# Performance work log

Hardware: AMD Instinct MI355X
Metric: run time of the kernel (lower is better)

## Reference

```python
import jax, jax.numpy as jnp
import numpy as np

STALK_DIM = 16
N_NODES = 50000
N_EDGES = 400000
HIDDEN = 64


def setup_inputs() -> dict:
    key = jax.random.key(0)
    k1, k2, k3, k4 = jax.random.split(key, 4)
    d = STALK_DIM
    x = jax.random.normal(k1, (N_NODES, d), dtype=jnp.float32)
    edge_index = jax.random.randint(k2, (2, N_EDGES), 0, N_NODES, dtype=jnp.int64)
    W1 = jax.random.normal(k3, (HIDDEN, 2 * d), dtype=jnp.float32) * (1.0 / np.sqrt(2 * d))
    b1 = jnp.zeros((HIDDEN,), dtype=jnp.float32)
    W2 = jax.random.normal(k4, (d, HIDDEN), dtype=jnp.float32) * (1.0 / np.sqrt(HIDDEN))
    b2 = jnp.zeros((d,), dtype=jnp.float32)
    return {"x": x, "edge_index": edge_index, "W1": W1, "b1": b1, "W2": W2, "b2": b2}


def reference(x, edge_index, W1, b1, W2, b2):
    d = x.shape[1]
    n = x.shape[0]
    src, dst = edge_index[0], edge_index[1]
    xs, xd = x[src], x[dst]  # [E, d]

    def reflection(a, b):
        h = jax.nn.relu(jnp.concatenate([a, b], axis=1) @ W1.T + b1)
        return h @ W2.T + b2  # [E, d]

    def householder(v):
        # F.normalize(v, dim=1): v / max(||v||, 1e-12)
        vn = v / jnp.maximum(jnp.linalg.norm(v, axis=1, keepdims=True), 1e-12)
        return jnp.eye(d, dtype=v.dtype)[None] - 2.0 * vn[:, :, None] * vn[:, None, :]

    F_s = householder(reflection(xs, xd))  # [E, d, d]
    F_d = householder(reflection(xd, xs))  # [E, d, d]
    L_sd = -jnp.einsum('eki,ekj->eij', F_s, F_d)  # -F_s^T @ F_d, [E, d, d]

    # degrees: both endpoints of every edge contribute 1
    ones_e = jnp.ones(src.shape[0], dtype=x.dtype)
    deg = jnp.zeros(n, dtype=x.dtype).at[src].add(ones_e).at[dst].add(ones_e)
    deg_inv_sqrt = 1.0 / jnp.sqrt(jnp.maximum(deg, 1e-5))
    # D_inv_sqrt is scalar*I per node, so normalization is a scalar coefficient per edge
    coef = deg_inv_sqrt[src] * deg_inv_sqrt[dst]  # [E]

    # out[s] -= D^-1/2_s L D^-1/2_d x[d] ; out[d] -= D^-1/2_d L^T D^-1/2_s x[s]
    msg_s = coef[:, None] * jnp.einsum('eij,ej->ei', L_sd, xd)  # goes to src
    msg_d = coef[:, None] * jnp.einsum('eji,ej->ei', L_sd, xs)  # goes to dst

    out = x - jnp.zeros_like(x).at[src].add(msg_s) - jnp.zeros_like(x).at[dst].add(msg_d)
    return jax.nn.relu(out)
```

## Files before the change

kernel.cpp:

```cpp
#include <hip/hip_runtime.h>
#include <hip/hip_bf16.h>

#define N_NODES 50000
#define N_EDGES 400000
#define D 16
#define HID 64

#define SCAN_B 256
#define SCAN_G ((N_NODES + SCAN_B - 1) / SCAN_B)

typedef unsigned short ushort_t;

#define CNT4_OFF  0
#define DEG_OFF   (4 * N_NODES)
#define OFF_OFF   (5 * N_NODES)
#define CUR_OFF   (6 * N_NODES + 1)
#define BS_OFF    (7 * N_NODES + 1)
#define FLAGS_I   (BS_OFF + SCAN_G)
#define MSG_OFF_I (((FLAGS_I + 2) + 3) & ~3)
#define CSR_NEEDED_BYTES ((size_t)(MSG_OFF_I + 2 * N_EDGES * D) * 4 + 64)

#define FB_NDEG   (N_NODES)
#define FB_NACC   (N_NODES * D)
#define FB_FLAGS  (FB_NDEG + FB_NACC)

__device__ __forceinline__ float bf_bits(ushort_t us) {
    return __uint_as_float(((unsigned)us) << 16);
}
__device__ __forceinline__ ushort_t f2bf(float v) {
    unsigned u = __float_as_uint(v);
    unsigned r = (u + 0x7fffu + ((u >> 16) & 1u)) >> 16;
    return (ushort_t)r;
}
__device__ __forceinline__ float ld_f(const void* p, int idx, int f32) {
    return f32 ? ((const float*)p)[idx]
               : bf_bits(((const ushort_t*)p)[idx]);
}

__device__ __forceinline__ void load16(const void* __restrict__ p, long long base,
                                       int f32, float* o) {
    if (f32) {
        const float4* q = (const float4*)((const float*)p + base);
        float4 a = q[0], b = q[1], c = q[2], d = q[3];
        o[0]=a.x; o[1]=a.y; o[2]=a.z; o[3]=a.w;
        o[4]=b.x; o[5]=b.y; o[6]=b.z; o[7]=b.w;
        o[8]=c.x; o[9]=c.y; o[10]=c.z; o[11]=c.w;
        o[12]=d.x; o[13]=d.y; o[14]=d.z; o[15]=d.w;
    } else {
        const uint4* q = (const uint4*)((const ushort_t*)p + base);
        uint4 a = q[0], b = q[1];
        unsigned u[8] = {a.x, a.y, a.z, a.w, b.x, b.y, b.z, b.w};
#pragma unroll
        for (int k = 0; k < 8; k++) {
            o[2 * k]     = __uint_as_float(u[k] << 16);
            o[2 * k + 1] = __uint_as_float(u[k] & 0xffff0000u);
        }
    }
}

__device__ __forceinline__ void load_edge(const void* __restrict__ ei, int e, int is64,
                                          int& s, int& d) {
    if (is64) {
        const long long* p = (const long long*)ei;
        s = (int)p[e];
        d = (int)p[N_EDGES + e];
    } else {
        const int* p = (const int*)ei;
        s = p[e];
        d = p[N_EDGES + e];
    }
}

__device__ __forceinline__ void detect_flags(const void* x, const void* ei, int* flags) {
    const ushort_t* h = (const ushort_t*)x;
    int f32 = 0;
    for (int k = 0; k < 256; k++) {
        float v = bf_bits(h[k]);
        if (!(v == v) || fabsf(v) > 1.0e6f) { f32 = 1; break; }
    }
    const long long* p = (const long long*)ei;
    int i64 = 1;
    for (int k = 0; k < 16; k++) {
        long long v = p[k];
        if (v < 0 || v >= N_NODES) { i64 = 0; break; }
    }
    flags[0] = f32;
    flags[1] = i64;
}

__device__ __forceinline__ void stage_weights(
    const void* W1, const void* b1, const void* W2, const void* b2, int f32,
    float* sW1, float* sW2t, float* sb1, float* sb2)
{
    int t = threadIdx.x;
    for (int idx = t; idx < HID * 2 * D; idx += blockDim.x)
        sW1[idx] = ld_f(W1, idx, f32);
    for (int idx = t; idx < HID * D; idx += blockDim.x) {
        int j = idx / D, i = idx % D;
        sW2t[idx] = ld_f(W2, i * HID + j, f32);
    }
    if (t < HID) sb1[t] = ld_f(b1, t, f32);
    if (t < D)  sb2[t] = ld_f(b2, t, f32);
}

__device__ __forceinline__ void edge_math_v4(
    const float* __restrict__ sW1, const float* __restrict__ sW2t,
    const float* __restrict__ sb1, const float* __restrict__ sb2,
    const float* xs, const float* xd, float coef,
    float* ms, float* md)
{
    float vs[D], vd[D];
#pragma unroll
    for (int i = 0; i < D; i++) { vs[i] = sb2[i]; vd[i] = sb2[i]; }

#pragma unroll 4
    for (int j = 0; j < HID; j++) {
        float hs = sb1[j], hd = sb1[j];
        const float4* w4 = (const float4*)&sW1[j * 2 * D];
#pragma unroll
        for (int t = 0; t < 4; t++) {
            float4 wv = w4[t];
            int k = 4 * t;
            hs = fmaf(wv.x, xs[k],     hs); hd = fmaf(wv.x, xd[k],     hd);
            hs = fmaf(wv.y, xs[k + 1], hs); hd = fmaf(wv.y, xd[k + 1], hd);
            hs = fmaf(wv.z, xs[k + 2], hs); hd = fmaf(wv.z, xd[k + 2], hd);
            hs = fmaf(wv.w, xs[k + 3], hs); hd = fmaf(wv.w, xd[k + 3], hd);
        }
#pragma unroll
        for (int t = 0; t < 4; t++) {
            float4 wv = w4[4 + t];
            int k = 4 * t;
            hs = fmaf(wv.x, xd[k],     hs); hd = fmaf(wv.x, xs[k],     hd);
            hs = fmaf(wv.y, xd[k + 1], hs); hd = fmaf(wv.y, xs[k + 1], hd);
            hs = fmaf(wv.z, xd[k + 2], hs); hd = fmaf(wv.z, xs[k + 2], hd);
            hs = fmaf(wv.w, xd[k + 3], hs); hd = fmaf(wv.w, xs[k + 3], hd);
        }
        hs = fmaxf(hs, 0.0f);
        hd = fmaxf(hd, 0.0f);
        const float4* w24 = (const float4*)&sW2t[j * D];
#pragma unroll
        for (int t = 0; t < 4; t++) {
            float4 u = w24[t];
            int i = 4 * t;
            vs[i]     = fmaf(u.x, hs, vs[i]);     vd[i]     = fmaf(u.x, hd, vd[i]);
            vs[i + 1] = fmaf(u.y, hs, vs[i + 1]); vd[i + 1] = fmaf(u.y, hd, vd[i + 1]);
            vs[i + 2] = fmaf(u.z, hs, vs[i + 2]); vd[i + 2] = fmaf(u.z, hd, vd[i + 2]);
            vs[i + 3] = fmaf(u.w, hs, vs[i + 3]); vd[i + 3] = fmaf(u.w, hd, vd[i + 3]);
        }
    }

    float ns = 0.0f, nd = 0.0f;
#pragma unroll
    for (int i = 0; i < D; i++) { ns = fmaf(vs[i], vs[i], ns); nd = fmaf(vd[i], vd[i], nd); }
    float is_ = 1.0f / fmaxf(sqrtf(ns), 1e-12f);
    float id_ = 1.0f / fmaxf(sqrtf(nd), 1e-12f);
#pragma unroll
    for (int i = 0; i < D; i++) { vs[i] *= is_; vd[i] *= id_; }

    float dot1 = 0.0f;
#pragma unroll
    for (int i = 0; i < D; i++) dot1 = fmaf(vd[i], xd[i], dot1);
#pragma unroll
    for (int i = 0; i < D; i++) ms[i] = fmaf(-2.0f * dot1, vd[i], xd[i]);
    float dot2 = 0.0f;
#pragma unroll
    for (int i = 0; i < D; i++) dot2 = fmaf(vs[i], ms[i], dot2);
#pragma unroll
    for (int i = 0; i < D; i++) ms[i] = coef * fmaf(-2.0f * dot2, vs[i], ms[i]);

    float dot3 = 0.0f;
#pragma unroll
    for (int i = 0; i < D; i++) dot3 = fmaf(vs[i], xs[i], dot3);
#pragma unroll
    for (int i = 0; i < D; i++) md[i] = fmaf(-2.0f * dot3, vs[i], xs[i]);
    float dot4 = 0.0f;
#pragma unroll
    for (int i = 0; i < D; i++) dot4 = fmaf(vd[i], md[i], dot4);
#pragma unroll
    for (int i = 0; i < D; i++) md[i] = coef * fmaf(-2.0f * dot4, vd[i], md[i]);
}

__global__ void csr_init_kernel(int* __restrict__ wsI,
                                const void* __restrict__ x,
                                const void* __restrict__ ei) {
    int i = blockIdx.x * blockDim.x + threadIdx.x;
    if (i < 4 * N_NODES) wsI[CNT4_OFF + i] = 0;
    if (blockIdx.x == 0 && threadIdx.x == 0)
        detect_flags(x, ei, wsI + FLAGS_I);
}

__global__ void csr_count_kernel(const void* __restrict__ ei, int* __restrict__ wsI) {
    int i64 = wsI[FLAGS_I + 1];
    int e = blockIdx.x * blockDim.x + threadIdx.x;
    if (e >= N_EDGES) return;
    int s, d;
    load_edge(ei, e, i64, s, d);
    int r = (e & 3) * N_NODES;
    atomicAdd(&wsI[CNT4_OFF + r + s], 1);
    atomicAdd(&wsI[CNT4_OFF + r + d], 1);
}

__global__ __launch_bounds__(SCAN_B) void csr_scan1_kernel(int* __restrict__ wsI) {
    __shared__ int sm[SCAN_B];
    int t = threadIdx.x;
    int g = blockIdx.x * SCAN_B + t;
    int c = 0;
    if (g < N_NODES) {
        c = wsI[CNT4_OFF + g] + wsI[CNT4_OFF + N_NODES + g]
          + wsI[CNT4_OFF + 2 * N_NODES + g] + wsI[CNT4_OFF + 3 * N_NODES + g];
        wsI[DEG_OFF + g] = c;
    }
    sm[t] = c;
    __syncthreads();
    for (int st = SCAN_B / 2; st > 0; st >>= 1) {
        if (t < st) sm[t] += sm[t + st];
        __syncthreads();
    }
    if (t == 0) wsI[BS_OFF + blockIdx.x] = sm[0];
}

__global__ __launch_bounds__(SCAN_B) void csr_scan3_kernel(int* __restrict__ wsI) {
    __shared__ int sB[SCAN_B];
    __shared__ int sm[SCAN_B];
    int t = threadIdx.x;
    int bsv = (t < SCAN_G) ? wsI[BS_OFF + t] : 0;
    sB[t] = bsv;
    __syncthreads();
    for (int st = 1; st < SCAN_B; st <<= 1) {
        int u = (t >= st) ? sB[t - st] : 0;
        __syncthreads();
        sB[t] += u;
        __syncthreads();
    }
    int blockBase = sB[blockIdx.x] - wsI[BS_OFF + blockIdx.x];

    int g = blockIdx.x * SCAN_B + t;
    int c = (g < N_NODES) ? wsI[DEG_OFF + g] : 0;
    sm[t] = c;
    __syncthreads();
    for (int st = 1; st < SCAN_B; st <<= 1) {
        int u = (t >= st) ? sm[t - st] : 0;
        __syncthreads();
        sm[t] += u;
        __syncthreads();
    }
    int excl = sm[t] - c + blockBase;
    if (g < N_NODES) {
        wsI[OFF_OFF + g] = excl;
        wsI[CUR_OFF + g] = excl;
        if (g == N_NODES - 1) wsI[OFF_OFF + N_NODES] = excl + c;
    }
}

__global__ __launch_bounds__(256) void csr_edge_kernel(
    const void* __restrict__ x,
    const void* __restrict__ ei,
    const void* __restrict__ W1,
    const void* __restrict__ b1,
    const void* __restrict__ W2,
    const void* __restrict__ b2,
    int* __restrict__ wsI)
{
    __shared__ __align__(16) float sW1[HID * 2 * D];
    __shared__ __align__(16) float sW2t[HID * D];
    __shared__ float sb1[HID];
    __shared__ float sb2[D];

    int f32 = wsI[FLAGS_I];
    int i64 = wsI[FLAGS_I + 1];
    stage_weights(W1, b1, W2, b2, f32, sW1, sW2t, sb1, sb2);
    __syncthreads();

    int e = blockIdx.x * blockDim.x + threadIdx.x;
    if (e >= N_EDGES) return;

    int s, d;
    load_edge(ei, e, i64, s, d);

    float xs[D], xd[D];
    load16(x, (long long)s * D, f32, xs);
    load16(x, (long long)d * D, f32, xd);

    float degs = (float)wsI[DEG_OFF + s];
    float degd = (float)wsI[DEG_OFF + d];
    float coef = (1.0f / sqrtf(fmaxf(degs, 1e-5f))) * (1.0f / sqrtf(fmaxf(degd, 1e-5f)));

    float ms[D], md[D];
    edge_math_v4(sW1, sW2t, sb1, sb2, xs, xd, coef, ms, md);

    float* msg = (float*)(wsI + MSG_OFF_I);
    int slot_s = atomicAdd(&wsI[CUR_OFF + s], 1);
    float4* m0 = (float4*)(msg + (long long)slot_s * D);
    m0[0] = make_float4(ms[0], ms[1], ms[2], ms[3]);
    m0[1] = make_float4(ms[4], ms[5], ms[6], ms[7]);
    m0[2] = make_float4(ms[8], ms[9], ms[10], ms[11]);
    m0[3] = make_float4(ms[12], ms[13], ms[14], ms[15]);
    int slot_d = atomicAdd(&wsI[CUR_OFF + d], 1);
    float4* m1 = (float4*)(msg + (long long)slot_d * D);
    m1[0] = make_float4(md[0], md[1], md[2], md[3]);
    m1[1] = make_float4(md[4], md[5], md[6], md[7]);
    m1[2] = make_float4(md[8], md[9], md[10], md[11]);
    m1[3] = make_float4(md[12], md[13], md[14], md[15]);
}

__global__ __launch_bounds__(256) void csr_gather_kernel(
    const void* __restrict__ x,
    const int* __restrict__ wsI,
    void* __restrict__ out)
{
    int f32 = wsI[FLAGS_I];
    int n = blockIdx.x * 64 + (threadIdx.x >> 2);
    int c = threadIdx.x & 3;
    if (n >= N_NODES) return;

    const int* off = wsI + OFF_OFF;
    const float4* msg4 = (const float4*)(wsI + MSG_OFF_I);

    int beg = off[n], end = off[n + 1];
    float4 a = make_float4(0.0f, 0.0f, 0.0f, 0.0f);
    int it = beg;
    for (; it + 2 <= end; it += 2) {
        float4 u = msg4[(long long)it * 4 + c];
        float4 v = msg4[(long long)(it + 1) * 4 + c];
        a.x += u.x + v.x; a.y += u.y + v.y; a.z += u.z + v.z; a.w += u.w + v.w;
    }
    if (it < end) {
        float4 u = msg4[(long long)it * 4 + c];
        a.x += u.x; a.y += u.y; a.z += u.z; a.w += u.w;
    }

    long long xb = (long long)n * D + 4 * c;
    float4 xv;
    if (f32) {
        xv = *(const float4*)((const float*)x + xb);
    } else {
        uint2 u = *(const uint2*)((const ushort_t*)x + xb);
        xv.x = __uint_as_float(u.x << 16);
        xv.y = __uint_as_float(u.x & 0xffff0000u);
        xv.z = __uint_as_float(u.y << 16);
        xv.w = __uint_as_float(u.y & 0xffff0000u);
    }
    float4 r;
    r.x = fmaxf(xv.x + a.x, 0.0f);
    r.y = fmaxf(xv.y + a.y, 0.0f);
    r.z = fmaxf(xv.z + a.z, 0.0f);
    r.w = fmaxf(xv.w + a.w, 0.0f);
    if (f32) {
        *(float4*)((float*)out + xb) = r;
    } else {
        uint2 o;
        o.x = (unsigned)f2bf(r.x) | ((unsigned)f2bf(r.y) << 16);
        o.y = (unsigned)f2bf(r.z) | ((unsigned)f2bf(r.w) << 16);
        *(uint2*)((ushort_t*)out + xb) = o;
    }
}

__global__ void fb_init_kernel(float* __restrict__ ws,
                               const void* __restrict__ x,
                               const void* __restrict__ ei) {
    int i = blockIdx.x * blockDim.x + threadIdx.x;
    if (i < FB_FLAGS) ws[i] = 0.0f;
    if (blockIdx.x == 0 && threadIdx.x == 0)
        detect_flags(x, ei, (int*)(ws + FB_FLAGS));
}

__global__ void fb_deg_kernel(const void* __restrict__ ei, float* __restrict__ ws) {
    int i64 = ((const int*)(ws + FB_FLAGS))[1];
    int e = blockIdx.x * blockDim.x + threadIdx.x;
    if (e >= N_EDGES) return;
    int s, d;
    load_edge(ei, e, i64, s, d);
    atomicAdd(&ws[s], 1.0f);
    atomicAdd(&ws[d], 1.0f);
}

__global__ __launch_bounds__(256) void fb_edge_kernel(
    const void* __restrict__ x, const void* __restrict__ ei,
    const void* __restrict__ W1, const void* __restrict__ b1,
    const void* __restrict__ W2, const void* __restrict__ b2,
    float* __restrict__ ws)
{
    __shared__ __align__(16) float sW1[HID * 2 * D];
    __shared__ __align__(16) float sW2t[HID * D];
    __shared__ float sb1[HID];
    __shared__ float sb2[D];
    const int* flags = (const int*)(ws + FB_FLAGS);
    int f32 = flags[0], i64 = flags[1];
    stage_weights(W1, b1, W2, b2, f32, sW1, sW2t, sb1, sb2);
    __syncthreads();
    int e = blockIdx.x * blockDim.x + threadIdx.x;
    if (e >= N_EDGES) return;
    int s, d;
    load_edge(ei, e, i64, s, d);
    float xs[D], xd[D];
    load16(x, (long long)s * D, f32, xs);
    load16(x, (long long)d * D, f32, xd);
    float coef = (1.0f / sqrtf(fmaxf(ws[s], 1e-5f))) * (1.0f / sqrtf(fmaxf(ws[d], 1e-5f)));
    float ms[D], md[D];
    edge_math_v4(sW1, sW2t, sb1, sb2, xs, xd, coef, ms, md);
    float* acc = ws + FB_NDEG;
#pragma unroll
    for (int i = 0; i < D; i++) atomicAdd(&acc[(long long)s * D + i], ms[i]);
#pragma unroll
    for (int i = 0; i < D; i++) atomicAdd(&acc[(long long)d * D + i], md[i]);
}

__global__ void fb_finalize_kernel(const void* __restrict__ x,
                                   const float* __restrict__ ws,
                                   void* __restrict__ out)
{
    int f32 = ((const int*)(ws + FB_FLAGS))[0];
    const float* acc = ws + FB_NDEG;
    int i = blockIdx.x * blockDim.x + threadIdx.x;
    if (i >= FB_NACC) return;
    float v = ld_f(x, i, f32) + acc[i];
    v = fmaxf(v, 0.0f);
    if (f32) ((float*)out)[i] = v;
    else     ((__hip_bfloat16*)out)[i] = __float2bfloat16(v);
}

extern "C" void kernel_launch(void* const* d_in, const int* in_sizes, int n_in,
                              void* d_out, int out_size, void* d_ws, size_t ws_size,
                              hipStream_t stream)
{
    const void* x  = d_in[0];
    const void* ei = d_in[1];
    const void* W1 = d_in[2];
    const void* b1 = d_in[3];
    const void* W2 = d_in[4];
    const void* b2 = d_in[5];

    int blk = 256;
    if (ws_size >= CSR_NEEDED_BYTES) {
        int* wsI = (int*)d_ws;
        csr_init_kernel<<<(4 * N_NODES + blk - 1) / blk, blk, 0, stream>>>(wsI, x, ei);
        csr_count_kernel<<<(N_EDGES + blk - 1) / blk, blk, 0, stream>>>(ei, wsI);
        csr_scan1_kernel<<<SCAN_G, SCAN_B, 0, stream>>>(wsI);
        csr_scan3_kernel<<<SCAN_G, SCAN_B, 0, stream>>>(wsI);
        csr_edge_kernel<<<(N_EDGES + blk - 1) / blk, blk, 0, stream>>>(x, ei, W1, b1, W2, b2, wsI);
        csr_gather_kernel<<<(N_NODES + 63) / 64, blk, 0, stream>>>(x, wsI, d_out);
    } else {
        float* ws = (float*)d_ws;
        fb_init_kernel<<<(FB_FLAGS + blk - 1) / blk, blk, 0, stream>>>(ws, x, ei);
        fb_deg_kernel<<<(N_EDGES + blk - 1) / blk, blk, 0, stream>>>(ei, ws);
        fb_edge_kernel<<<(N_EDGES + blk - 1) / blk, blk, 0, stream>>>(x, ei, W1, b1, W2, b2, ws);
        fb_finalize_kernel<<<(FB_NACC + blk - 1) / blk, blk, 0, stream>>>(x, ws, d_out);
    }
}
```

Before: 201.4 us.

## Precompute per-node first-layer projections and factor Householder messages in bf16 path

```diff
diff --git a/kernel.cpp b/kernel.cpp
--- a/kernel.cpp
+++ b/kernel.cpp
@@ -8,6 +8,8 @@
 
 #define SCAN_B 256
 #define SCAN_G ((N_NODES + SCAN_B - 1) / SCAN_B)
+#define NB_E ((N_EDGES + 255) / 256)
+#define NB_G ((2 * N_NODES + 255) / 256)
 
 typedef unsigned short ushort_t;
 
@@ -16,8 +18,8 @@
 #define OFF_OFF   (5 * N_NODES)
 #define CUR_OFF   (6 * N_NODES + 1)
 #define BS_OFF    (7 * N_NODES + 1)
-#define FLAGS_I   (BS_OFF + SCAN_G)
-#define MSG_OFF_I (((FLAGS_I + 2) + 3) & ~3)
+#define MSG_OFF_I (((BS_OFF + SCAN_G) + 3) & ~3)
+#define G_OFF     (MSG_OFF_I + 2 * N_EDGES * 8)
 #define CSR_NEEDED_BYTES ((size_t)(MSG_OFF_I + 2 * N_EDGES * D) * 4 + 64)
 
 #define FB_NDEG   (N_NODES)
@@ -27,6 +29,8 @@
 __device__ __forceinline__ float bf_bits(ushort_t us) {
     return __uint_as_float(((unsigned)us) << 16);
 }
+__device__ __forceinline__ float lo_bf(unsigned u) { return __uint_as_float(u << 16); }
+__device__ __forceinline__ float hi_bf(unsigned u) { return __uint_as_float(u & 0xffff0000u); }
 __device__ __forceinline__ ushort_t f2bf(float v) {
     unsigned u = __float_as_uint(v);
     unsigned r = (u + 0x7fffu + ((u >> 16) & 1u)) >> 16;
@@ -52,8 +56,8 @@
         unsigned u[8] = {a.x, a.y, a.z, a.w, b.x, b.y, b.z, b.w};
 #pragma unroll
         for (int k = 0; k < 8; k++) {
-            o[2 * k]     = __uint_as_float(u[k] << 16);
-            o[2 * k + 1] = __uint_as_float(u[k] & 0xffff0000u);
+            o[2 * k]     = lo_bf(u[k]);
+            o[2 * k + 1] = hi_bf(u[k]);
         }
     }
 }
@@ -86,21 +90,6 @@
     }
     flags[0] = f32;
     flags[1] = i64;
-}
-
-__device__ __forceinline__ void stage_weights(
-    const void* W1, const void* b1, const void* W2, const void* b2, int f32,
-    float* sW1, float* sW2t, float* sb1, float* sb2)
-{
-    int t = threadIdx.x;
-    for (int idx = t; idx < HID * 2 * D; idx += blockDim.x)
-        sW1[idx] = ld_f(W1, idx, f32);
-    for (int idx = t; idx < HID * D; idx += blockDim.x) {
-        int j = idx / D, i = idx % D;
-        sW2t[idx] = ld_f(W2, i * HID + j, f32);
-    }
-    if (t < HID) sb1[t] = ld_f(b1, t, f32);
-    if (t < D)  sb2[t] = ld_f(b2, t, f32);
 }
 
 __device__ __forceinline__ void edge_math_v4(
@@ -180,24 +169,74 @@
     for (int i = 0; i < D; i++) md[i] = coef * fmaf(-2.0f * dot4, vd[i], md[i]);
 }
 
-__global__ void csr_init_kernel(int* __restrict__ wsI,
-                                const void* __restrict__ x,
-                                const void* __restrict__ ei) {
-    int i = blockIdx.x * blockDim.x + threadIdx.x;
-    if (i < 4 * N_NODES) wsI[CNT4_OFF + i] = 0;
-    if (blockIdx.x == 0 && threadIdx.x == 0)
-        detect_flags(x, ei, wsI + FLAGS_I);
-}
-
-__global__ void csr_count_kernel(const void* __restrict__ ei, int* __restrict__ wsI) {
-    int i64 = wsI[FLAGS_I + 1];
-    int e = blockIdx.x * blockDim.x + threadIdx.x;
-    if (e >= N_EDGES) return;
-    int s, d;
-    load_edge(ei, e, i64, s, d);
-    int r = (e & 3) * N_NODES;
-    atomicAdd(&wsI[CNT4_OFF + r + s], 1);
-    atomicAdd(&wsI[CNT4_OFF + r + d], 1);
+
+__global__ __launch_bounds__(256) void csr_count_gprep_kernel(
+    const void* __restrict__ ei,
+    const void* __restrict__ x,
+    const void* __restrict__ W1,
+    int* __restrict__ wsI)
+{
+    __shared__ int sfl[2];
+    __shared__ __align__(16) float sW1[HID * 32];
+    if (threadIdx.x == 0) detect_flags(x, ei, sfl);
+    __syncthreads();
+    int f32 = sfl[0], i64 = sfl[1];
+
+    if (blockIdx.x < NB_E) {
+        int e = blockIdx.x * 256 + threadIdx.x;
+        if (e >= N_EDGES) return;
+        int s, d;
+        load_edge(ei, e, i64, s, d);
+        int r = (e & 3) * N_NODES;
+        atomicAdd(&wsI[CNT4_OFF + r + s], 1);
+        atomicAdd(&wsI[CNT4_OFF + r + d], 1);
+    } else {
+        if (f32) return;
+        for (int idx = threadIdx.x; idx < HID * 32; idx += 256)
+            sW1[idx] = ld_f(W1, idx, 0);
+        __syncthreads();
+        int idx = (blockIdx.x - NB_E) * 256 + threadIdx.x;
+        if (idx >= 2 * N_NODES) return;
+        int n = idx >> 1, half = idx & 1;
+        float xv[D];
+        load16(x, (long long)n * D, 0, xv);
+        unsigned pk[8];
+#pragma unroll 4
+        for (int j0 = 0; j0 < HID; j0 += 2) {
+            float d0 = 0.0f, d1 = 0.0f;
+            const float* w0 = &sW1[j0 * 32 + half * 16];
+            const float* w1 = w0 + 32;
+#pragma unroll
+            for (int k = 0; k < D; k++) {
+                d0 = fmaf(w0[k], xv[k], d0);
+                d1 = fmaf(w1[k], xv[k], d1);
+            }
+            pk[(j0 >> 3)] = (j0 & 4)
+                ? (pk[(j0 >> 3)] & 0xffffffffu)
+                : pk[(j0 >> 3)];
+            unsigned w = (unsigned)f2bf(d0) | ((unsigned)f2bf(d1) << 16);
+            ((unsigned*)pk)[j0 >> 1] = w;
+        }
+        ushort_t* gout = (ushort_t*)(wsI + G_OFF) + (long long)n * 128 + half * 64;
+        uint4* g4 = (uint4*)gout;
+        g4[0] = make_uint4(((unsigned*)pk)[0], ((unsigned*)pk)[1], ((unsigned*)pk)[2], ((unsigned*)pk)[3]);
+        g4[1] = make_uint4(((unsigned*)pk)[4], ((unsigned*)pk)[5], ((unsigned*)pk)[6], ((unsigned*)pk)[7]);
+        unsigned pk2[8];
+#pragma unroll 4
+        for (int j0 = 32; j0 < HID; j0 += 2) {
+            float d0 = 0.0f, d1 = 0.0f;
+            const float* w0 = &sW1[j0 * 32 + half * 16];
+            const float* w1 = w0 + 32;
+#pragma unroll
+            for (int k = 0; k < D; k++) {
+                d0 = fmaf(w0[k], xv[k], d0);
+                d1 = fmaf(w1[k], xv[k], d1);
+            }
+            ((unsigned*)pk2)[(j0 - 32) >> 1] = (unsigned)f2bf(d0) | ((unsigned)f2bf(d1) << 16);
+        }
+        g4[2] = make_uint4(((unsigned*)pk2)[0], ((unsigned*)pk2)[1], ((unsigned*)pk2)[2], ((unsigned*)pk2)[3]);
+        g4[3] = make_uint4(((unsigned*)pk2)[4], ((unsigned*)pk2)[5], ((unsigned*)pk2)[6], ((unsigned*)pk2)[7]);
+    }
 }
 
 __global__ __launch_bounds__(SCAN_B) void csr_scan1_kernel(int* __restrict__ wsI) {
@@ -261,72 +300,204 @@
     const void* __restrict__ b2,
     int* __restrict__ wsI)
 {
-    __shared__ __align__(16) float sW1[HID * 2 * D];
     __shared__ __align__(16) float sW2t[HID * D];
     __shared__ float sb1[HID];
     __shared__ float sb2[D];
-
-    int f32 = wsI[FLAGS_I];
-    int i64 = wsI[FLAGS_I + 1];
-    stage_weights(W1, b1, W2, b2, f32, sW1, sW2t, sb1, sb2);
-    __syncthreads();
-
-    int e = blockIdx.x * blockDim.x + threadIdx.x;
+    __shared__ __align__(16) float sW1f[HID * 2 * D];
+    __shared__ int sfl[2];
+
+    if (threadIdx.x == 0) detect_flags(x, ei, sfl);
+    __syncthreads();
+    int f32 = sfl[0], i64 = sfl[1];
+
+    int t = threadIdx.x;
+    for (int idx = t; idx < HID * D; idx += 256) {
+        int j = idx / D, i = idx % D;
+        sW2t[idx] = ld_f(W2, i * HID + j, f32);
+    }
+    if (t < HID) sb1[t] = ld_f(b1, t, f32);
+    if (t < D)  sb2[t] = ld_f(b2, t, f32);
+    if (f32) {
+        for (int idx = t; idx < HID * 2 * D; idx += 256)
+            sW1f[idx] = ld_f(W1, idx, 1);
+    }
+    __syncthreads();
+
+    int e = blockIdx.x * 256 + t;
     if (e >= N_EDGES) return;
 
     int s, d;
     load_edge(ei, e, i64, s, d);
-
-    float xs[D], xd[D];
-    load16(x, (long long)s * D, f32, xs);
-    load16(x, (long long)d * D, f32, xd);
-
     float degs = (float)wsI[DEG_OFF + s];
     float degd = (float)wsI[DEG_OFF + d];
     float coef = (1.0f / sqrtf(fmaxf(degs, 1e-5f))) * (1.0f / sqrtf(fmaxf(degd, 1e-5f)));
 
-    float ms[D], md[D];
-    edge_math_v4(sW1, sW2t, sb1, sb2, xs, xd, coef, ms, md);
-
-    float* msg = (float*)(wsI + MSG_OFF_I);
-    int slot_s = atomicAdd(&wsI[CUR_OFF + s], 1);
-    float4* m0 = (float4*)(msg + (long long)slot_s * D);
-    m0[0] = make_float4(ms[0], ms[1], ms[2], ms[3]);
-    m0[1] = make_float4(ms[4], ms[5], ms[6], ms[7]);
-    m0[2] = make_float4(ms[8], ms[9], ms[10], ms[11]);
-    m0[3] = make_float4(ms[12], ms[13], ms[14], ms[15]);
-    int slot_d = atomicAdd(&wsI[CUR_OFF + d], 1);
-    float4* m1 = (float4*)(msg + (long long)slot_d * D);
-    m1[0] = make_float4(md[0], md[1], md[2], md[3]);
-    m1[1] = make_float4(md[4], md[5], md[6], md[7]);
-    m1[2] = make_float4(md[8], md[9], md[10], md[11]);
-    m1[3] = make_float4(md[12], md[13], md[14], md[15]);
+    if (!f32) {
+        const ushort_t* g = (const ushort_t*)(wsI + G_OFF);
+        const ushort_t* gS = g + (long long)s * 128;
+        const ushort_t* gD = g + (long long)d * 128;
+
+        float vs[D], vd[D];
+#pragma unroll
+        for (int i = 0; i < D; i++) { vs[i] = sb2[i]; vd[i] = sb2[i]; }
+
+        for (int jj = 0; jj < HID; jj += 8) {
+            uint4 u1s = *(const uint4*)(gS + jj);
+            uint4 u2s = *(const uint4*)(gS + 64 + jj);
+            uint4 u1d = *(const uint4*)(gD + jj);
+            uint4 u2d = *(const uint4*)(gD + 64 + jj);
+            unsigned w1s[4] = {u1s.x, u1s.y, u1s.z, u1s.w};
+            unsigned w2s[4] = {u2s.x, u2s.y, u2s.z, u2s.w};
+            unsigned w1d[4] = {u1d.x, u1d.y, u1d.z, u1d.w};
+            unsigned w2d[4] = {u2d.x, u2d.y, u2d.z, u2d.w};
+#pragma unroll
+            for (int w = 0; w < 4; w++) {
+#pragma unroll
+                for (int sub = 0; sub < 2; sub++) {
+                    int j = jj + 2 * w + sub;
+                    float g1s = sub ? hi_bf(w1s[w]) : lo_bf(w1s[w]);
+                    float g2s = sub ? hi_bf(w2s[w]) : lo_bf(w2s[w]);
+                    float g1d = sub ? hi_bf(w1d[w]) : lo_bf(w1d[w]);
+                    float g2d = sub ? hi_bf(w2d[w]) : lo_bf(w2d[w]);
+                    float bj = sb1[j];
+                    float hs = fmaxf(g1s + g2d + bj, 0.0f);
+                    float hd = fmaxf(g1d + g2s + bj, 0.0f);
+                    const float4* w24 = (const float4*)&sW2t[j * D];
+#pragma unroll
+                    for (int tt = 0; tt < 4; tt++) {
+                        float4 u = w24[tt];
+                        int i = 4 * tt;
+                        vs[i]     = fmaf(u.x, hs, vs[i]);     vd[i]     = fmaf(u.x, hd, vd[i]);
+                        vs[i + 1] = fmaf(u.y, hs, vs[i + 1]); vd[i + 1] = fmaf(u.y, hd, vd[i + 1]);
+                        vs[i + 2] = fmaf(u.z, hs, vs[i + 2]); vd[i + 2] = fmaf(u.z, hd, vd[i + 2]);
+                        vs[i + 3] = fmaf(u.w, hs, vs[i + 3]); vd[i + 3] = fmaf(u.w, hd, vd[i + 3]);
+                    }
+                }
+            }
+        }
+
+        float ns = 0.0f, nd = 0.0f;
+#pragma unroll
+        for (int i = 0; i < D; i++) { ns = fmaf(vs[i], vs[i], ns); nd = fmaf(vd[i], vd[i], nd); }
+        float is_ = 1.0f / fmaxf(sqrtf(ns), 1e-12f);
+        float id_ = 1.0f / fmaxf(sqrtf(nd), 1e-12f);
+#pragma unroll
+        for (int i = 0; i < D; i++) { vs[i] *= is_; vd[i] *= id_; }
+        float c = 0.0f;
+#pragma unroll
+        for (int i = 0; i < D; i++) c = fmaf(vs[i], vd[i], c);
+
+        ushort_t* msgh = (ushort_t*)(wsI + MSG_OFF_I);
+        float xv[D];
+
+        load16(x, (long long)d * D, 0, xv);
+        float a = 0.0f, b = 0.0f;
+#pragma unroll
+        for (int i = 0; i < D; i++) { a = fmaf(vd[i], xv[i], a); b = fmaf(vs[i], xv[i], b); }
+        float k2 = -2.0f * a * coef;
+        float k3 = -2.0f * (b - 2.0f * a * c) * coef;
+        int slot_s = atomicAdd(&wsI[CUR_OFF + s], 1);
+        {
+            unsigned pk[8];
+#pragma unroll
+            for (int i = 0; i < D; i += 2) {
+                float m0 = fmaf(coef, xv[i],     fmaf(k2, vd[i],     k3 * vs[i]));
+                float m1 = fmaf(coef, xv[i + 1], fmaf(k2, vd[i + 1], k3 * vs[i + 1]));
+                pk[i >> 1] = (unsigned)f2bf(m0) | ((unsigned)f2bf(m1) << 16);
+            }
+            uint4* mp = (uint4*)(msgh + (long long)slot_s * D);
+            mp[0] = make_uint4(pk[0], pk[1], pk[2], pk[3]);
+            mp[1] = make_uint4(pk[4], pk[5], pk[6], pk[7]);
+        }
+
+        load16(x, (long long)s * D, 0, xv);
+        float a2 = 0.0f, b2v = 0.0f;
+#pragma unroll
+        for (int i = 0; i < D; i++) { a2 = fmaf(vs[i], xv[i], a2); b2v = fmaf(vd[i], xv[i], b2v); }
+        float k2b = -2.0f * a2 * coef;
+        float k3b = -2.0f * (b2v - 2.0f * a2 * c) * coef;
+        int slot_d = atomicAdd(&wsI[CUR_OFF + d], 1);
+        {
+            unsigned pk[8];
+#pragma unroll
+            for (int i = 0; i < D; i += 2) {
+                float m0 = fmaf(coef, xv[i],     fmaf(k2b, vs[i],     k3b * vd[i]));
+                float m1 = fmaf(coef, xv[i + 1], fmaf(k2b, vs[i + 1], k3b * vd[i + 1]));
+                pk[i >> 1] = (unsigned)f2bf(m0) | ((unsigned)f2bf(m1) << 16);
+            }
+            uint4* mp = (uint4*)(msgh + (long long)slot_d * D);
+            mp[0] = make_uint4(pk[0], pk[1], pk[2], pk[3]);
+            mp[1] = make_uint4(pk[4], pk[5], pk[6], pk[7]);
+        }
+    } else {
+        float xs[D], xd[D];
+        load16(x, (long long)s * D, 1, xs);
+        load16(x, (long long)d * D, 1, xd);
+        float ms[D], md[D];
+        edge_math_v4(sW1f, sW2t, sb1, sb2, xs, xd, coef, ms, md);
+        float* msg = (float*)(wsI + MSG_OFF_I);
+        int slot_s = atomicAdd(&wsI[CUR_OFF + s], 1);
+        float4* m0 = (float4*)(msg + (long long)slot_s * D);
+        m0[0] = make_float4(ms[0], ms[1], ms[2], ms[3]);
+        m0[1] = make_float4(ms[4], ms[5], ms[6], ms[7]);
+        m0[2] = make_float4(ms[8], ms[9], ms[10], ms[11]);
+        m0[3] = make_float4(ms[12], ms[13], ms[14], ms[15]);
+        int slot_d = atomicAdd(&wsI[CUR_OFF + d], 1);
+        float4* m1 = (float4*)(msg + (long long)slot_d * D);
+        m1[0] = make_float4(md[0], md[1], md[2], md[3]);
+        m1[1] = make_float4(md[4], md[5], md[6], md[7]);
+        m1[2] = make_float4(md[8], md[9], md[10], md[11]);
+        m1[3] = make_float4(md[12], md[13], md[14], md[15]);
+    }
 }
 
 __global__ __launch_bounds__(256) void csr_gather_kernel(
     const void* __restrict__ x,
+    const void* __restrict__ ei,
     const int* __restrict__ wsI,
     void* __restrict__ out)
 {
-    int f32 = wsI[FLAGS_I];
+    __shared__ int sfl[2];
+    if (threadIdx.x == 0) detect_flags(x, ei, sfl);
+    __syncthreads();
+    int f32 = sfl[0];
+
     int n = blockIdx.x * 64 + (threadIdx.x >> 2);
     int c = threadIdx.x & 3;
     if (n >= N_NODES) return;
 
     const int* off = wsI + OFF_OFF;
-    const float4* msg4 = (const float4*)(wsI + MSG_OFF_I);
-
     int beg = off[n], end = off[n + 1];
+
     float4 a = make_float4(0.0f, 0.0f, 0.0f, 0.0f);
-    int it = beg;
-    for (; it + 2 <= end; it += 2) {
-        float4 u = msg4[(long long)it * 4 + c];
-        float4 v = msg4[(long long)(it + 1) * 4 + c];
-        a.x += u.x + v.x; a.y += u.y + v.y; a.z += u.z + v.z; a.w += u.w + v.w;
-    }
-    if (it < end) {
-        float4 u = msg4[(long long)it * 4 + c];
-        a.x += u.x; a.y += u.y; a.z += u.z; a.w += u.w;
+    if (f32) {
+        const float4* msg4 = (const float4*)(wsI + MSG_OFF_I);
+        int it = beg;
+        for (; it + 2 <= end; it += 2) {
+            float4 u = msg4[(long long)it * 4 + c];
+            float4 v = msg4[(long long)(it + 1) * 4 + c];
+            a.x += u.x + v.x; a.y += u.y + v.y; a.z += u.z + v.z; a.w += u.w + v.w;
+        }
+        if (it < end) {
+            float4 u = msg4[(long long)it * 4 + c];
+            a.x += u.x; a.y += u.y; a.z += u.z; a.w += u.w;
+        }
+    } else {
+        const ushort_t* msgh = (const ushort_t*)(wsI + MSG_OFF_I);
+        int it = beg;
+        for (; it + 2 <= end; it += 2) {
+            uint2 u = *(const uint2*)(msgh + (long long)it * D + 4 * c);
+            uint2 v = *(const uint2*)(msgh + (long long)(it + 1) * D + 4 * c);
+            a.x += lo_bf(u.x) + lo_bf(v.x);
+            a.y += hi_bf(u.x) + hi_bf(v.x);
+            a.z += lo_bf(u.y) + lo_bf(v.y);
+            a.w += hi_bf(u.y) + hi_bf(v.y);
+        }
+        if (it < end) {
+            uint2 u = *(const uint2*)(msgh + (long long)it * D + 4 * c);
+            a.x += lo_bf(u.x); a.y += hi_bf(u.x);
+            a.z += lo_bf(u.y); a.w += hi_bf(u.y);
+        }
     }
 
     long long xb = (long long)n * D + 4 * c;
@@ -335,10 +506,8 @@
         xv = *(const float4*)((const float*)x + xb);
     } else {
         uint2 u = *(const uint2*)((const ushort_t*)x + xb);
-        xv.x = __uint_as_float(u.x << 16);
-        xv.y = __uint_as_float(u.x & 0xffff0000u);
-        xv.z = __uint_as_float(u.y << 16);
-        xv.w = __uint_as_float(u.y & 0xffff0000u);
+        xv.x = lo_bf(u.x); xv.y = hi_bf(u.x);
+        xv.z = lo_bf(u.y); xv.w = hi_bf(u.y);
     }
     float4 r;
     r.x = fmaxf(xv.x + a.x, 0.0f);
@@ -353,6 +522,21 @@
         o.y = (unsigned)f2bf(r.z) | ((unsigned)f2bf(r.w) << 16);
         *(uint2*)((ushort_t*)out + xb) = o;
     }
+}
+
+__device__ __forceinline__ void stage_weights(
+    const void* W1, const void* b1, const void* W2, const void* b2, int f32,
+    float* sW1, float* sW2t, float* sb1, float* sb2)
+{
+    int t = threadIdx.x;
+    for (int idx = t; idx < HID * 2 * D; idx += blockDim.x)
+        sW1[idx] = ld_f(W1, idx, f32);
+    for (int idx = t; idx < HID * D; idx += blockDim.x) {
+        int j = idx / D, i = idx % D;
+        sW2t[idx] = ld_f(W2, i * HID + j, f32);
+    }
+    if (t < HID) sb1[t] = ld_f(b1, t, f32);
+    if (t < D)  sb2[t] = ld_f(b2, t, f32);
 }
 
 __global__ void fb_init_kernel(float* __restrict__ ws,
@@ -433,12 +617,12 @@
     int blk = 256;
     if (ws_size >= CSR_NEEDED_BYTES) {
         int* wsI = (int*)d_ws;
-        csr_init_kernel<<<(4 * N_NODES + blk - 1) / blk, blk, 0, stream>>>(wsI, x, ei);
-        csr_count_kernel<<<(N_EDGES + blk - 1) / blk, blk, 0, stream>>>(ei, wsI);
+        hipMemsetAsync(d_ws, 0, (size_t)4 * N_NODES * sizeof(int), stream);
+        csr_count_gprep_kernel<<<NB_E + NB_G, blk, 0, stream>>>(ei, x, W1, wsI);
         csr_scan1_kernel<<<SCAN_G, SCAN_B, 0, stream>>>(wsI);
         csr_scan3_kernel<<<SCAN_G, SCAN_B, 0, stream>>>(wsI);
-        csr_edge_kernel<<<(N_EDGES + blk - 1) / blk, blk, 0, stream>>>(x, ei, W1, b1, W2, b2, wsI);
-        csr_gather_kernel<<<(N_NODES + 63) / 64, blk, 0, stream>>>(x, wsI, d_out);
+        csr_edge_kernel<<<NB_E, blk, 0, stream>>>(x, ei, W1, b1, W2, b2, wsI);
+        csr_gather_kernel<<<(N_NODES + 63) / 64, blk, 0, stream>>>(x, ei, wsI, d_out);
     } else {
         float* ws = (float*)d_ws;
         fb_init_kernel<<<(FB_FLAGS + blk - 1) / blk, blk, 0, stream>>>(ws, x, ei);
```

Result: slower. 224.2 us (+11.4%).

## Process two edges per thread, store bf16 messages, drop init kernel

Applied to the files above, without the earlier changes.

```diff
diff --git a/kernel.cpp b/kernel.cpp
--- a/kernel.cpp
+++ b/kernel.cpp
@@ -8,6 +8,7 @@
 
 #define SCAN_B 256
 #define SCAN_G ((N_NODES + SCAN_B - 1) / SCAN_B)
+#define NB_E2 ((N_EDGES + 511) / 512)
 
 typedef unsigned short ushort_t;
 
@@ -16,8 +17,7 @@
 #define OFF_OFF   (5 * N_NODES)
 #define CUR_OFF   (6 * N_NODES + 1)
 #define BS_OFF    (7 * N_NODES + 1)
-#define FLAGS_I   (BS_OFF + SCAN_G)
-#define MSG_OFF_I (((FLAGS_I + 2) + 3) & ~3)
+#define MSG_OFF_I (((BS_OFF + SCAN_G) + 3) & ~3)
 #define CSR_NEEDED_BYTES ((size_t)(MSG_OFF_I + 2 * N_EDGES * D) * 4 + 64)
 
 #define FB_NDEG   (N_NODES)
@@ -27,6 +27,8 @@
 __device__ __forceinline__ float bf_bits(ushort_t us) {
     return __uint_as_float(((unsigned)us) << 16);
 }
+__device__ __forceinline__ float lo_bf(unsigned u) { return __uint_as_float(u << 16); }
+__device__ __forceinline__ float hi_bf(unsigned u) { return __uint_as_float(u & 0xffff0000u); }
 __device__ __forceinline__ ushort_t f2bf(float v) {
     unsigned u = __float_as_uint(v);
     unsigned r = (u + 0x7fffu + ((u >> 16) & 1u)) >> 16;
@@ -52,8 +54,8 @@
         unsigned u[8] = {a.x, a.y, a.z, a.w, b.x, b.y, b.z, b.w};
 #pragma unroll
         for (int k = 0; k < 8; k++) {
-            o[2 * k]     = __uint_as_float(u[k] << 16);
-            o[2 * k + 1] = __uint_as_float(u[k] & 0xffff0000u);
+            o[2 * k]     = lo_bf(u[k]);
+            o[2 * k + 1] = hi_bf(u[k]);
         }
     }
 }
@@ -112,7 +114,6 @@
     float vs[D], vd[D];
 #pragma unroll
     for (int i = 0; i < D; i++) { vs[i] = sb2[i]; vd[i] = sb2[i]; }
-
 #pragma unroll 4
     for (int j = 0; j < HID; j++) {
         float hs = sb1[j], hd = sb1[j];
@@ -148,7 +149,6 @@
             vs[i + 3] = fmaf(u.w, hs, vs[i + 3]); vd[i + 3] = fmaf(u.w, hd, vd[i + 3]);
         }
     }
-
     float ns = 0.0f, nd = 0.0f;
 #pragma unroll
     for (int i = 0; i < D; i++) { ns = fmaf(vs[i], vs[i], ns); nd = fmaf(vd[i], vd[i], nd); }
@@ -156,7 +156,6 @@
     float id_ = 1.0f / fmaxf(sqrtf(nd), 1e-12f);
 #pragma unroll
     for (int i = 0; i < D; i++) { vs[i] *= is_; vd[i] *= id_; }
-
     float dot1 = 0.0f;
 #pragma unroll
     for (int i = 0; i < D; i++) dot1 = fmaf(vd[i], xd[i], dot1);
@@ -167,7 +166,6 @@
     for (int i = 0; i < D; i++) dot2 = fmaf(vs[i], ms[i], dot2);
 #pragma unroll
     for (int i = 0; i < D; i++) ms[i] = coef * fmaf(-2.0f * dot2, vs[i], ms[i]);
-
     float dot3 = 0.0f;
 #pragma unroll
     for (int i = 0; i < D; i++) dot3 = fmaf(vs[i], xs[i], dot3);
@@ -180,17 +178,13 @@
     for (int i = 0; i < D; i++) md[i] = coef * fmaf(-2.0f * dot4, vd[i], md[i]);
 }
 
-__global__ void csr_init_kernel(int* __restrict__ wsI,
-                                const void* __restrict__ x,
-                                const void* __restrict__ ei) {
-    int i = blockIdx.x * blockDim.x + threadIdx.x;
-    if (i < 4 * N_NODES) wsI[CNT4_OFF + i] = 0;
-    if (blockIdx.x == 0 && threadIdx.x == 0)
-        detect_flags(x, ei, wsI + FLAGS_I);
-}
-
-__global__ void csr_count_kernel(const void* __restrict__ ei, int* __restrict__ wsI) {
-    int i64 = wsI[FLAGS_I + 1];
+__global__ void csr_count_kernel(const void* __restrict__ ei,
+                                 const void* __restrict__ x,
+                                 int* __restrict__ wsI) {
+    __shared__ int sfl[2];
+    if (threadIdx.x == 0) detect_flags(x, ei, sfl);
+    __syncthreads();
+    int i64 = sfl[1];
     int e = blockIdx.x * blockDim.x + threadIdx.x;
     if (e >= N_EDGES) return;
     int s, d;
@@ -252,7 +246,76 @@
     }
 }
 
-__global__ __launch_bounds__(256) void csr_edge_kernel(
+__device__ __forceinline__ void edge_epilogue(
+    float* vs, float* vd, const float* xs, const float* xd,
+    int s, int d, float coef, int active, int f32, int* __restrict__ wsI)
+{
+    float ns = 0.0f, nd = 0.0f;
+#pragma unroll
+    for (int i = 0; i < D; i++) { ns = fmaf(vs[i], vs[i], ns); nd = fmaf(vd[i], vd[i], nd); }
+    float is_ = 1.0f / fmaxf(sqrtf(ns), 1e-12f);
+    float id_ = 1.0f / fmaxf(sqrtf(nd), 1e-12f);
+#pragma unroll
+    for (int i = 0; i < D; i++) { vs[i] *= is_; vd[i] *= id_; }
+
+    float ms[D], md[D];
+    float dot1 = 0.0f;
+#pragma unroll
+    for (int i = 0; i < D; i++) dot1 = fmaf(vd[i], xd[i], dot1);
+#pragma unroll
+    for (int i = 0; i < D; i++) ms[i] = fmaf(-2.0f * dot1, vd[i], xd[i]);
+    float dot2 = 0.0f;
+#pragma unroll
+    for (int i = 0; i < D; i++) dot2 = fmaf(vs[i], ms[i], dot2);
+#pragma unroll
+    for (int i = 0; i < D; i++) ms[i] = coef * fmaf(-2.0f * dot2, vs[i], ms[i]);
+    float dot3 = 0.0f;
+#pragma unroll
+    for (int i = 0; i < D; i++) dot3 = fmaf(vs[i], xs[i], dot3);
+#pragma unroll
+    for (int i = 0; i < D; i++) md[i] = fmaf(-2.0f * dot3, vs[i], xs[i]);
+    float dot4 = 0.0f;
+#pragma unroll
+    for (int i = 0; i < D; i++) dot4 = fmaf(vd[i], md[i], dot4);
+#pragma unroll
+    for (int i = 0; i < D; i++) md[i] = coef * fmaf(-2.0f * dot4, vd[i], md[i]);
+
+    if (!active) return;
+    if (f32) {
+        float* msg = (float*)(wsI + MSG_OFF_I);
+        int slot_s = atomicAdd(&wsI[CUR_OFF + s], 1);
+        float4* m0 = (float4*)(msg + (long long)slot_s * D);
+        m0[0] = make_float4(ms[0], ms[1], ms[2], ms[3]);
+        m0[1] = make_float4(ms[4], ms[5], ms[6], ms[7]);
+        m0[2] = make_float4(ms[8], ms[9], ms[10], ms[11]);
+        m0[3] = make_float4(ms[12], ms[13], ms[14], ms[15]);
+        int slot_d = atomicAdd(&wsI[CUR_OFF + d], 1);
+        float4* m1 = (float4*)(msg + (long long)slot_d * D);
+        m1[0] = make_float4(md[0], md[1], md[2], md[3]);
+        m1[1] = make_float4(md[4], md[5], md[6], md[7]);
+        m1[2] = make_float4(md[8], md[9], md[10], md[11]);
+        m1[3] = make_float4(md[12], md[13], md[14], md[15]);
+    } else {
+        ushort_t* msgh = (ushort_t*)(wsI + MSG_OFF_I);
+        unsigned pk[8];
+#pragma unroll
+        for (int i = 0; i < D; i += 2)
+            pk[i >> 1] = (unsigned)f2bf(ms[i]) | ((unsigned)f2bf(ms[i + 1]) << 16);
+        int slot_s = atomicAdd(&wsI[CUR_OFF + s], 1);
+        uint4* mp = (uint4*)(msgh + (long long)slot_s * D);
+        mp[0] = make_uint4(pk[0], pk[1], pk[2], pk[3]);
+        mp[1] = make_uint4(pk[4], pk[5], pk[6], pk[7]);
+#pragma unroll
+        for (int i = 0; i < D; i += 2)
+            pk[i >> 1] = (unsigned)f2bf(md[i]) | ((unsigned)f2bf(md[i + 1]) << 16);
+        int slot_d = atomicAdd(&wsI[CUR_OFF + d], 1);
+        uint4* mq = (uint4*)(msgh + (long long)slot_d * D);
+        mq[0] = make_uint4(pk[0], pk[1], pk[2], pk[3]);
+        mq[1] = make_uint4(pk[4], pk[5], pk[6], pk[7]);
+    }
+}
+
+__global__ __launch_bounds__(256, 2) void csr_edge2_kernel(
     const void* __restrict__ x,
     const void* __restrict__ ei,
     const void* __restrict__ W1,
@@ -265,68 +328,146 @@
     __shared__ __align__(16) float sW2t[HID * D];
     __shared__ float sb1[HID];
     __shared__ float sb2[D];
-
-    int f32 = wsI[FLAGS_I];
-    int i64 = wsI[FLAGS_I + 1];
+    __shared__ int sfl[2];
+
+    if (threadIdx.x == 0) detect_flags(x, ei, sfl);
+    __syncthreads();
+    int f32 = sfl[0], i64 = sfl[1];
     stage_weights(W1, b1, W2, b2, f32, sW1, sW2t, sb1, sb2);
     __syncthreads();
 
-    int e = blockIdx.x * blockDim.x + threadIdx.x;
-    if (e >= N_EDGES) return;
-
-    int s, d;
-    load_edge(ei, e, i64, s, d);
-
-    float xs[D], xd[D];
-    load16(x, (long long)s * D, f32, xs);
-    load16(x, (long long)d * D, f32, xd);
-
-    float degs = (float)wsI[DEG_OFF + s];
-    float degd = (float)wsI[DEG_OFF + d];
-    float coef = (1.0f / sqrtf(fmaxf(degs, 1e-5f))) * (1.0f / sqrtf(fmaxf(degd, 1e-5f)));
-
-    float ms[D], md[D];
-    edge_math_v4(sW1, sW2t, sb1, sb2, xs, xd, coef, ms, md);
-
-    float* msg = (float*)(wsI + MSG_OFF_I);
-    int slot_s = atomicAdd(&wsI[CUR_OFF + s], 1);
-    float4* m0 = (float4*)(msg + (long long)slot_s * D);
-    m0[0] = make_float4(ms[0], ms[1], ms[2], ms[3]);
-    m0[1] = make_float4(ms[4], ms[5], ms[6], ms[7]);
-    m0[2] = make_float4(ms[8], ms[9], ms[10], ms[11]);
-    m0[3] = make_float4(ms[12], ms[13], ms[14], ms[15]);
-    int slot_d = atomicAdd(&wsI[CUR_OFF + d], 1);
-    float4* m1 = (float4*)(msg + (long long)slot_d * D);
-    m1[0] = make_float4(md[0], md[1], md[2], md[3]);
-    m1[1] = make_float4(md[4], md[5], md[6], md[7]);
-    m1[2] = make_float4(md[8], md[9], md[10], md[11]);
-    m1[3] = make_float4(md[12], md[13], md[14], md[15]);
+    int t = threadIdx.x;
+    int e0 = blockIdx.x * 512 + t;
+    int e1 = e0 + 256;
+    int act0 = e0 < N_EDGES;
+    int act1 = e1 < N_EDGES;
+    int c0 = act0 ? e0 : 0;
+    int c1 = act1 ? e1 : 0;
+
+    int s0, d0, s1, d1;
+    load_edge(ei, c0, i64, s0, d0);
+    load_edge(ei, c1, i64, s1, d1);
+
+    float degs0 = (float)wsI[DEG_OFF + s0];
+    float degd0 = (float)wsI[DEG_OFF + d0];
+    float degs1 = (float)wsI[DEG_OFF + s1];
+    float degd1 = (float)wsI[DEG_OFF + d1];
+    float coef0 = (1.0f / sqrtf(fmaxf(degs0, 1e-5f))) * (1.0f / sqrtf(fmaxf(degd0, 1e-5f)));
+    float coef1 = (1.0f / sqrtf(fmaxf(degs1, 1e-5f))) * (1.0f / sqrtf(fmaxf(degd1, 1e-5f)));
+
+    float xs0[D], xd0[D], xs1[D], xd1[D];
+    load16(x, (long long)s0 * D, f32, xs0);
+    load16(x, (long long)d0 * D, f32, xd0);
+    load16(x, (long long)s1 * D, f32, xs1);
+    load16(x, (long long)d1 * D, f32, xd1);
+
+    float vs0[D], vd0[D], vs1[D], vd1[D];
+#pragma unroll
+    for (int i = 0; i < D; i++) {
+        float b = sb2[i];
+        vs0[i] = b; vd0[i] = b; vs1[i] = b; vd1[i] = b;
+    }
+
+#pragma unroll 2
+    for (int j = 0; j < HID; j++) {
+        float bj = sb1[j];
+        float hs0 = bj, hd0 = bj, hs1 = bj, hd1 = bj;
+        const float4* w4 = (const float4*)&sW1[j * 2 * D];
+#pragma unroll
+        for (int tt = 0; tt < 4; tt++) {
+            float4 wv = w4[tt];
+            int k = 4 * tt;
+            hs0 = fmaf(wv.x, xs0[k],     hs0); hd0 = fmaf(wv.x, xd0[k],     hd0);
+            hs1 = fmaf(wv.x, xs1[k],     hs1); hd1 = fmaf(wv.x, xd1[k],     hd1);
+            hs0 = fmaf(wv.y, xs0[k + 1], hs0); hd0 = fmaf(wv.y, xd0[k + 1], hd0);
+            hs1 = fmaf(wv.y, xs1[k + 1], hs1); hd1 = fmaf(wv.y, xd1[k + 1], hd1);
+            hs0 = fmaf(wv.z, xs0[k + 2], hs0); hd0 = fmaf(wv.z, xd0[k + 2], hd0);
+            hs1 = fmaf(wv.z, xs1[k + 2], hs1); hd1 = fmaf(wv.z, xd1[k + 2], hd1);
+            hs0 = fmaf(wv.w, xs0[k + 3], hs0); hd0 = fmaf(wv.w, xd0[k + 3], hd0);
+            hs1 = fmaf(wv.w, xs1[k + 3], hs1); hd1 = fmaf(wv.w, xd1[k + 3], hd1);
+        }
+#pragma unroll
+        for (int tt = 0; tt < 4; tt++) {
+            float4 wv = w4[4 + tt];
+            int k = 4 * tt;
+            hs0 = fmaf(wv.x, xd0[k],     hs0); hd0 = fmaf(wv.x, xs0[k],     hd0);
+            hs1 = fmaf(wv.x, xd1[k],     hs1); hd1 = fmaf(wv.x, xs1[k],     hd1);
+            hs0 = fmaf(wv.y, xd0[k + 1], hs0); hd0 = fmaf(wv.y, xs0[k + 1], hd0);
+            hs1 = fmaf(wv.y, xd1[k + 1], hs1); hd1 = fmaf(wv.y, xs1[k + 1], hd1);
+            hs0 = fmaf(wv.z, xd0[k + 2], hs0); hd0 = fmaf(wv.z, xs0[k + 2], hd0);
+            hs1 = fmaf(wv.z, xd1[k + 2], hs1); hd1 = fmaf(wv.z, xs1[k + 2], hd1);
+            hs0 = fmaf(wv.w, xd0[k + 3], hs0); hd0 = fmaf(wv.w, xs0[k + 3], hd0);
+            hs1 = fmaf(wv.w, xd1[k + 3], hs1); hd1 = fmaf(wv.w, xs1[k + 3], hd1);
+        }
+        hs0 = fmaxf(hs0, 0.0f); hd0 = fmaxf(hd0, 0.0f);
+        hs1 = fmaxf(hs1, 0.0f); hd1 = fmaxf(hd1, 0.0f);
+        const float4* w24 = (const float4*)&sW2t[j * D];
+#pragma unroll
+        for (int tt = 0; tt < 4; tt++) {
+            float4 u = w24[tt];
+            int i = 4 * tt;
+            vs0[i]     = fmaf(u.x, hs0, vs0[i]);     vd0[i]     = fmaf(u.x, hd0, vd0[i]);
+            vs1[i]     = fmaf(u.x, hs1, vs1[i]);     vd1[i]     = fmaf(u.x, hd1, vd1[i]);
+            vs0[i + 1] = fmaf(u.y, hs0, vs0[i + 1]); vd0[i + 1] = fmaf(u.y, hd0, vd0[i + 1]);
+            vs1[i + 1] = fmaf(u.y, hs1, vs1[i + 1]); vd1[i + 1] = fmaf(u.y, hd1, vd1[i + 1]);
+            vs0[i + 2] = fmaf(u.z, hs0, vs0[i + 2]); vd0[i + 2] = fmaf(u.z, hd0, vd0[i + 2]);
+            vs1[i + 2] = fmaf(u.z, hs1, vs1[i + 2]); vd1[i + 2] = fmaf(u.z, hd1, vd1[i + 2]);
+            vs0[i + 3] = fmaf(u.w, hs0, vs0[i + 3]); vd0[i + 3] = fmaf(u.w, hd0, vd0[i + 3]);
+            vs1[i + 3] = fmaf(u.w, hs1, vs1[i + 3]); vd1[i + 3] = fmaf(u.w, hd1, vd1[i + 3]);
+        }
+    }
+
+    edge_epilogue(vs0, vd0, xs0, xd0, s0, d0, coef0, act0, f32, wsI);
+    edge_epilogue(vs1, vd1, xs1, xd1, s1, d1, coef1, act1, f32, wsI);
 }
 
 __global__ __launch_bounds__(256) void csr_gather_kernel(
     const void* __restrict__ x,
+    const void* __restrict__ ei,
     const int* __restrict__ wsI,
     void* __restrict__ out)
 {
-    int f32 = wsI[FLAGS_I];
+    __shared__ int sfl[2];
+    if (threadIdx.x == 0) detect_flags(x, ei, sfl);
+    __syncthreads();
+    int f32 = sfl[0];
+
     int n = blockIdx.x * 64 + (threadIdx.x >> 2);
     int c = threadIdx.x & 3;
     if (n >= N_NODES) return;
 
     const int* off = wsI + OFF_OFF;
-    const float4* msg4 = (const float4*)(wsI + MSG_OFF_I);
-
     int beg = off[n], end = off[n + 1];
+
     float4 a = make_float4(0.0f, 0.0f, 0.0f, 0.0f);
-    int it = beg;
-    for (; it + 2 <= end; it += 2) {
-        float4 u = msg4[(long long)it * 4 + c];
-        float4 v = msg4[(long long)(it + 1) * 4 + c];
-        a.x += u.x + v.x; a.y += u.y + v.y; a.z += u.z + v.z; a.w += u.w + v.w;
-    }
-    if (it < end) {
-        float4 u = msg4[(long long)it * 4 + c];
-        a.x += u.x; a.y += u.y; a.z += u.z; a.w += u.w;
+    if (f32) {
+        const float4* msg4 = (const float4*)(wsI + MSG_OFF_I);
+        int it = beg;
+        for (; it + 2 <= end; it += 2) {
+            float4 u = msg4[(long long)it * 4 + c];
+            float4 v = msg4[(long long)(it + 1) * 4 + c];
+            a.x += u.x + v.x; a.y += u.y + v.y; a.z += u.z + v.z; a.w += u.w + v.w;
+        }
+        if (it < end) {
+            float4 u = msg4[(long long)it * 4 + c];
+            a.x += u.x; a.y += u.y; a.z += u.z; a.w += u.w;
+        }
+    } else {
+        const ushort_t* msgh = (const ushort_t*)(wsI + MSG_OFF_I);
+        int it = beg;
+        for (; it + 2 <= end; it += 2) {
+            uint2 u = *(const uint2*)(msgh + (long long)it * D + 4 * c);
+            uint2 v = *(const uint2*)(msgh + (long long)(it + 1) * D + 4 * c);
+            a.x += lo_bf(u.x) + lo_bf(v.x);
+            a.y += hi_bf(u.x) + hi_bf(v.x);
+            a.z += lo_bf(u.y) + lo_bf(v.y);
+            a.w += hi_bf(u.y) + hi_bf(v.y);
+        }
+        if (it < end) {
+            uint2 u = *(const uint2*)(msgh + (long long)it * D + 4 * c);
+            a.x += lo_bf(u.x); a.y += hi_bf(u.x);
+            a.z += lo_bf(u.y); a.w += hi_bf(u.y);
+        }
     }
 
     long long xb = (long long)n * D + 4 * c;
@@ -335,10 +476,8 @@
         xv = *(const float4*)((const float*)x + xb);
     } else {
         uint2 u = *(const uint2*)((const ushort_t*)x + xb);
-        xv.x = __uint_as_float(u.x << 16);
-        xv.y = __uint_as_float(u.x & 0xffff0000u);
-        xv.z = __uint_as_float(u.y << 16);
-        xv.w = __uint_as_float(u.y & 0xffff0000u);
+        xv.x = lo_bf(u.x); xv.y = hi_bf(u.x);
+        xv.z = lo_bf(u.y); xv.w = hi_bf(u.y);
     }
     float4 r;
     r.x = fmaxf(xv.x + a.x, 0.0f);
@@ -433,12 +572,12 @@
     int blk = 256;
     if (ws_size >= CSR_NEEDED_BYTES) {
         int* wsI = (int*)d_ws;
-        csr_init_kernel<<<(4 * N_NODES + blk - 1) / blk, blk, 0, stream>>>(wsI, x, ei);
-        csr_count_kernel<<<(N_EDGES + blk - 1) / blk, blk, 0, stream>>>(ei, wsI);
+        hipMemsetAsync(d_ws, 0, (size_t)4 * N_NODES * sizeof(int), stream);
+        csr_count_kernel<<<(N_EDGES + blk - 1) / blk, blk, 0, stream>>>(ei, x, wsI);
         csr_scan1_kernel<<<SCAN_G, SCAN_B, 0, stream>>>(wsI);
         csr_scan3_kernel<<<SCAN_G, SCAN_B, 0, stream>>>(wsI);
-        csr_edge_kernel<<<(N_EDGES + blk - 1) / blk, blk, 0, stream>>>(x, ei, W1, b1, W2, b2, wsI);
-        csr_gather_kernel<<<(N_NODES + 63) / 64, blk, 0, stream>>>(x, wsI, d_out);
+        csr_edge2_kernel<<<NB_E2, blk, 0, stream>>>(x, ei, W1, b1, W2, b2, wsI);
+        csr_gather_kernel<<<(N_NODES + 63) / 64, blk, 0, stream>>>(x, ei, wsI, d_out);
     } else {
         float* ws = (float*)d_ws;
         fb_init_kernel<<<(FB_FLAGS + blk - 1) / blk, blk, 0, stream>>>(ws, x, ei);
```

Result: slower. 236.4 us (+17.4%).
